# Optimization experiments

Hardware: AMD Instinct MI355X
Metric: run time of the kernel (lower is better)

## Reference

```python
import jax, jax.numpy as jnp
import numpy as np

B, IN_DIM, UNITS = 2048, 256, 512

def setup_inputs() -> dict:
    key = jax.random.key(0)
    k1, k2 = jax.random.split(key)
    x = jax.random.uniform(k1, (B, IN_DIM), dtype=jnp.float32)
    weights = jax.random.uniform(k2, (IN_DIM * UNITS,), dtype=jnp.float32)
    return {"x": x, "weights": weights}

def reference(x, weights):
    # kernel: [in_dim, units]; transpose -> [units, in_dim]
    in_dim = x.shape[-1]
    kT = weights.reshape(in_dim, UNITS).T  # [units, in_dim]
    # broadcast multiply-add: [B, 1, in_dim] * [units, in_dim] + (1 - kT)
    # -> [B, units, in_dim]; product-reduce over in_dim (XOR via bipolar product)
    t = x[:, None, :] * kT + (1.0 - kT)
    return jnp.prod(t, axis=-1)  # [B, units]
```

## Files before the change

### kernel.cpp

```cpp
#include <hip/hip_runtime.h>


typedef float v2f __attribute__((ext_vector_type(2)));

#define B_DIM   2048
#define IN_DIM  256
#define UNITS   512
#define BT      32
#define UT      64
#define BLOCK   256
#define NSL     8
#define KIS     32
#define CHUNK   8
#define NCH     4
#define PSTR    68
#define PLANE   (32*PSTR)

__global__ __launch_bounds__(BLOCK) void prodw_kernel(
    const float* __restrict__ x,
    const float* __restrict__ w,
    float* __restrict__ out)
{
    __shared__ __align__(16) float lds[4 * PLANE];
    float* __restrict__ xs  = lds;
    float* __restrict__ wsb = lds + 2048;

    const int tid = threadIdx.x;
    const int s   = tid >> 5;
    const int t   = tid & 31;
    const int tb  = t >> 3;
    const int tu  = t & 7;
    const int ublk = blockIdx.x * UT;
    const int bblk = blockIdx.y * BT;

    __align__(16) float af[64];
    v2f* __restrict__ acc = (v2f*)af;
#pragma unroll
    for (int k = 0; k < 32; ++k) acc[k] = (v2f){1.0f, 1.0f};

    const int swz = (s & 1) << 2;

    for (int c = 0; c < NCH; ++c) {
        __syncthreads();

#pragma unroll
        for (int r = 0; r < 2; ++r) {
            const int idx  = r * BLOCK + tid;
            const int b    = idx & 31;
            const int srow = idx >> 5;
            const int ss   = srow >> 1;
            const int h    = srow & 1;
            const float4 f = *(const float4*)
                (x + (size_t)(bblk + b) * IN_DIM + ss * KIS + c * CHUNK + h * 4);
            const int row = ss * 8 + h * 4;
            xs[(row + 0) * 32 + b] = f.x;
            xs[(row + 1) * 32 + b] = f.y;
            xs[(row + 2) * 32 + b] = f.z;
            xs[(row + 3) * 32 + b] = f.w;
        }
#pragma unroll
        for (int r = 0; r < 4; ++r) {
            const int idx = r * BLOCK + tid;
            const int row = idx >> 4;
            const int u4  = (idx & 15) * 4;
            const int ss  = row >> 3;
            const int ii  = row & 7;
            const int xr  = (ss & 1) << 2;
            const float4 f = *(const float4*)
                (w + (size_t)(ss * KIS + c * CHUNK + ii) * UNITS + ublk + u4);
            *(float4*)&wsb[row * 64 + (u4 ^ xr)] = f;
        }
        __syncthreads();

#pragma unroll
        for (int ii = 0; ii < CHUNK; ++ii) {
            const int row = s * 8 + ii;
            const float4 xa = *(const float4*)&xs[row * 32 + tb * 8];
            const float4 xb = *(const float4*)&xs[row * 32 + tb * 8 + 4];
            const float4 w0 = *(const float4*)&wsb[row * 64 + ((tu * 8) ^ swz)];
            const float4 w1 = *(const float4*)&wsb[row * 64 + ((tu * 8 + 4) ^ swz)];

            v2f wv[4] = {{w0.x, w0.y}, {w0.z, w0.w}, {w1.x, w1.y}, {w1.z, w1.w}};
            v2f cv[4];
#pragma unroll
            for (int q = 0; q < 4; ++q) cv[q] = (v2f){1.0f, 1.0f} - wv[q];
            const float xv[8] = {xa.x, xa.y, xa.z, xa.w, xb.x, xb.y, xb.z, xb.w};

#pragma unroll
            for (int jb = 0; jb < 8; ++jb) {
                const v2f xbv = {xv[jb], xv[jb]};
#pragma unroll
                for (int q = 0; q < 4; ++q)
                    acc[jb * 4 + q] *= __builtin_elementwise_fma(xbv, wv[q], cv[q]);
            }
        }
    }

#pragma unroll
    for (int half = NSL / 2; half >= 1; half >>= 1) {
        __syncthreads();
        if (s >= half && s < 2 * half) {
            float* __restrict__ pl = lds + (size_t)(s - half) * PLANE + t * PSTR;
#pragma unroll
            for (int k = 0; k < 16; ++k)
                *(float4*)&pl[k * 4] = ((const float4*)af)[k];
        }
        __syncthreads();
        if (s < half) {
            const float* __restrict__ pl = lds + (size_t)s * PLANE + t * PSTR;
#pragma unroll
            for (int k = 0; k < 16; ++k) {
                const float4 q = *(const float4*)&pl[k * 4];
                float4* a4 = &((float4*)af)[k];
                a4->x *= q.x; a4->y *= q.y; a4->z *= q.z; a4->w *= q.w;
            }
        }
    }

    if (s == 0) {
#pragma unroll
        for (int jb = 0; jb < 8; ++jb) {
            float* __restrict__ po =
                out + (size_t)(bblk + tb * 8 + jb) * UNITS + ublk + tu * 8;
            *(float4*)(po)     = *(const float4*)&af[jb * 8];
            *(float4*)(po + 4) = *(const float4*)&af[jb * 8 + 4];
        }
    }
}

extern "C" void kernel_launch(void* const* d_in, const int* in_sizes, int n_in,
                              void* d_out, int out_size, void* d_ws, size_t ws_size,
                              hipStream_t stream) {
    const float* x = (const float*)d_in[0];
    const float* w = (const float*)d_in[1];
    float* out     = (float*)d_out;

    dim3 grid(UNITS / UT, B_DIM / BT);
    prodw_kernel<<<grid, BLOCK, 0, stream>>>(x, w, out);
}
```

Before: 73.19 us.

## Double-buffer weight tiles via async global_load_lds and preload shifted x tile

Weight chunks now go straight from global memory into one of two LDS buffers using async global-to-LDS loads, and the next chunk is prefetched while the current one is computed. The whole x tile for the block is loaded into LDS once, before the loop, with 1 subtracted up front. Each factor then becomes fma(x-1, w, 1), so the per-chunk 1-w computation goes away and the per-chunk barriers drop from two to one. LDS use grows to 64KB per block, which can lower occupancy. Correctness relies on the async LDS writes having finished before the barrier.

```diff
diff --git a/kernel.cpp b/kernel.cpp
--- a/kernel.cpp
+++ b/kernel.cpp
@@ -16,33 +16,51 @@
 #define PSTR    68
 #define PLANE   (32*PSTR)
 
+#define XS_F    (IN_DIM*32)
+#define WBUF_F  (64*64)
+
 __global__ __launch_bounds__(BLOCK) void prodw_kernel(
     const float* __restrict__ x,
     const float* __restrict__ w,
     float* __restrict__ out)
 {
-    __shared__ __align__(16) float lds[4 * PLANE];
+    __shared__ __align__(16) float lds[XS_F + 2 * WBUF_F];
     float* __restrict__ xs  = lds;
-    float* __restrict__ wsb = lds + 2048;
+    float* __restrict__ ws0 = lds + XS_F;
+    float* __restrict__ ws1 = lds + XS_F + WBUF_F;
 
     const int tid = threadIdx.x;
     const int s   = tid >> 5;
     const int t   = tid & 31;
     const int tb  = t >> 3;
     const int tu  = t & 7;
+    const int wv  = tid >> 6;
+    const int ln  = tid & 63;
     const int ublk = blockIdx.x * UT;
     const int bblk = blockIdx.y * BT;
 
-    __align__(16) float af[64];
-    v2f* __restrict__ acc = (v2f*)af;
+    const float* wsrc[4];
+    int lofs[4];
 #pragma unroll
-    for (int k = 0; k < 32; ++k) acc[k] = (v2f){1.0f, 1.0f};
+    for (int k = 0; k < 4; ++k) {
+        const int seg = wv * 4 + k;
+        const int r   = seg * 4 + (ln >> 4);
+        const int ss  = r >> 3;
+        const int ii  = r & 7;
+        const int xr  = (ss & 1) << 2;
+        const int col = ((ln & 15) * 4) ^ xr;
+        wsrc[k] = w + (size_t)(ss * KIS + ii) * UNITS + ublk + col;
+        lofs[k] = seg * 256;
+    }
 
-    const int swz = (s & 1) << 2;
+#pragma unroll
+    for (int k = 0; k < 4; ++k)
+        __builtin_amdgcn_global_load_lds(
+            (const __attribute__((address_space(1))) void*)(wsrc[k]),
+            (__attribute__((address_space(3))) void*)(ws0 + lofs[k]), 16, 0, 0);
 
+#pragma unroll
     for (int c = 0; c < NCH; ++c) {
-        __syncthreads();
-
 #pragma unroll
         for (int r = 0; r < 2; ++r) {
             const int idx  = r * BLOCK + tid;
@@ -52,48 +70,60 @@
             const int h    = srow & 1;
             const float4 f = *(const float4*)
                 (x + (size_t)(bblk + b) * IN_DIM + ss * KIS + c * CHUNK + h * 4);
-            const int row = ss * 8 + h * 4;
-            xs[(row + 0) * 32 + b] = f.x;
-            xs[(row + 1) * 32 + b] = f.y;
-            xs[(row + 2) * 32 + b] = f.z;
-            xs[(row + 3) * 32 + b] = f.w;
+            const int row = ss * KIS + c * CHUNK + h * 4;
+            xs[(row + 0) * 32 + b] = f.x - 1.0f;
+            xs[(row + 1) * 32 + b] = f.y - 1.0f;
+            xs[(row + 2) * 32 + b] = f.z - 1.0f;
+            xs[(row + 3) * 32 + b] = f.w - 1.0f;
         }
+    }
+
+    __align__(16) float af[64];
+    v2f* __restrict__ acc = (v2f*)af;
 #pragma unroll
-        for (int r = 0; r < 4; ++r) {
-            const int idx = r * BLOCK + tid;
-            const int row = idx >> 4;
-            const int u4  = (idx & 15) * 4;
-            const int ss  = row >> 3;
-            const int ii  = row & 7;
-            const int xr  = (ss & 1) << 2;
-            const float4 f = *(const float4*)
-                (w + (size_t)(ss * KIS + c * CHUNK + ii) * UNITS + ublk + u4);
-            *(float4*)&wsb[row * 64 + (u4 ^ xr)] = f;
+    for (int k = 0; k < 32; ++k) acc[k] = (v2f){1.0f, 1.0f};
+
+    const int swz = (s & 1) << 2;
+
+    __syncthreads();
+
+#pragma unroll
+    for (int c = 0; c < NCH; ++c) {
+        float* const wcur = (c & 1) ? ws1 : ws0;
+        float* const wnxt = (c & 1) ? ws0 : ws1;
+
+        if (c + 1 < NCH) {
+            const size_t coff = (size_t)(c + 1) * CHUNK * UNITS;
+#pragma unroll
+            for (int k = 0; k < 4; ++k)
+                __builtin_amdgcn_global_load_lds(
+                    (const __attribute__((address_space(1))) void*)(wsrc[k] + coff),
+                    (__attribute__((address_space(3))) void*)(wnxt + lofs[k]),
+                    16, 0, 0);
         }
-        __syncthreads();
 
 #pragma unroll
         for (int ii = 0; ii < CHUNK; ++ii) {
-            const int row = s * 8 + ii;
-            const float4 xa = *(const float4*)&xs[row * 32 + tb * 8];
-            const float4 xb = *(const float4*)&xs[row * 32 + tb * 8 + 4];
-            const float4 w0 = *(const float4*)&wsb[row * 64 + ((tu * 8) ^ swz)];
-            const float4 w1 = *(const float4*)&wsb[row * 64 + ((tu * 8 + 4) ^ swz)];
+            const int xrow = s * KIS + c * CHUNK + ii;
+            const int wrow = s * CHUNK + ii;
+            const float4 ya = *(const float4*)&xs[xrow * 32 + tb * 8];
+            const float4 yb = *(const float4*)&xs[xrow * 32 + tb * 8 + 4];
+            const float4 w0 = *(const float4*)&wcur[wrow * 64 + ((tu * 8) ^ swz)];
+            const float4 w1 = *(const float4*)&wcur[wrow * 64 + ((tu * 8 + 4) ^ swz)];
 
-            v2f wv[4] = {{w0.x, w0.y}, {w0.z, w0.w}, {w1.x, w1.y}, {w1.z, w1.w}};
-            v2f cv[4];
-#pragma unroll
-            for (int q = 0; q < 4; ++q) cv[q] = (v2f){1.0f, 1.0f} - wv[q];
-            const float xv[8] = {xa.x, xa.y, xa.z, xa.w, xb.x, xb.y, xb.z, xb.w};
+            v2f wvv[4] = {{w0.x, w0.y}, {w0.z, w0.w}, {w1.x, w1.y}, {w1.z, w1.w}};
+            const float yv[8] = {ya.x, ya.y, ya.z, ya.w, yb.x, yb.y, yb.z, yb.w};
 
 #pragma unroll
             for (int jb = 0; jb < 8; ++jb) {
-                const v2f xbv = {xv[jb], xv[jb]};
+                const v2f yy = {yv[jb], yv[jb]};
 #pragma unroll
                 for (int q = 0; q < 4; ++q)
-                    acc[jb * 4 + q] *= __builtin_elementwise_fma(xbv, wv[q], cv[q]);
+                    acc[jb * 4 + q] *= __builtin_elementwise_fma(
+                        yy, wvv[q], (v2f){1.0f, 1.0f});
             }
         }
+        __syncthreads();
     }
 
 #pragma unroll
```

New measurement: 71.76 us. 1.02x faster.

## Use per-wave k-slices with wave-uniform weight loads and fma(w, x-1, 1)

Applied to the files above, without the earlier changes.

Rewrites the kernel so each of 16 waves owns a 16-wide slice of in_dim, with each lane handling one batch row and holding x-1 in registers. Weights are read directly from global memory at wave-uniform addresses (scalar-loadable) instead of being staged through LDS. The factor becomes fma(w, x-1, 1), which removes the per-element 1-w computation. Block size grows to 1024 threads with 64x64 tiles, and a 4-level LDS tree reduction with an XOR swizzle combines the partial products. The trade-off is a larger reduction, fewer blocks, and possible register pressure from 64 accumulators per lane under a 1024-thread launch bound.

```diff
diff --git a/kernel.cpp b/kernel.cpp
--- a/kernel.cpp
+++ b/kernel.cpp
@@ -6,125 +6,82 @@
 #define B_DIM   2048
 #define IN_DIM  256
 #define UNITS   512
-#define BT      32
+#define BT      64
 #define UT      64
-#define BLOCK   256
-#define NSL     8
-#define KIS     32
-#define CHUNK   8
-#define NCH     4
-#define PSTR    68
-#define PLANE   (32*PSTR)
+#define BLOCK   1024
+#define NW      16
+#define KIS     16
+#define PLANE_F (64*64)
 
-__global__ __launch_bounds__(BLOCK) void prodw_kernel(
+__global__ __launch_bounds__(BLOCK, 4) void prodw_kernel(
     const float* __restrict__ x,
     const float* __restrict__ w,
     float* __restrict__ out)
 {
-    __shared__ __align__(16) float lds[4 * PLANE];
-    float* __restrict__ xs  = lds;
-    float* __restrict__ wsb = lds + 2048;
+    __shared__ __align__(16) float lds[(NW / 2) * PLANE_F];
 
-    const int tid = threadIdx.x;
-    const int s   = tid >> 5;
-    const int t   = tid & 31;
-    const int tb  = t >> 3;
-    const int tu  = t & 7;
+    const int tid  = threadIdx.x;
+    const int ln   = tid & 63;
+    const int wid  = __builtin_amdgcn_readfirstlane(tid >> 6);
     const int ublk = blockIdx.x * UT;
     const int bblk = blockIdx.y * BT;
 
-    __align__(16) float af[64];
-    v2f* __restrict__ acc = (v2f*)af;
+    float yv[KIS];
+    {
+        const float* xp = x + (size_t)(bblk + ln) * IN_DIM + wid * KIS;
 #pragma unroll
-    for (int k = 0; k < 32; ++k) acc[k] = (v2f){1.0f, 1.0f};
+        for (int k = 0; k < KIS / 4; ++k) {
+            const float4 f = *(const float4*)(xp + 4 * k);
+            yv[4 * k + 0] = f.x - 1.0f;
+            yv[4 * k + 1] = f.y - 1.0f;
+            yv[4 * k + 2] = f.z - 1.0f;
+            yv[4 * k + 3] = f.w - 1.0f;
+        }
+    }
 
-    const int swz = (s & 1) << 2;
+    v2f acc[32];
+#pragma unroll
+    for (int q = 0; q < 32; ++q) acc[q] = (v2f){1.0f, 1.0f};
 
-    for (int c = 0; c < NCH; ++c) {
-        __syncthreads();
+    const float* wp = w + (size_t)(wid * KIS) * UNITS + ublk;
+
+#pragma unroll 4
+    for (int ii = 0; ii < KIS; ++ii) {
+        const float* wr = wp + (size_t)ii * UNITS;
+        const v2f yy = {yv[ii], yv[ii]};
+#pragma unroll
+        for (int q = 0; q < 32; ++q) {
+            const v2f wv = *(const v2f*)(wr + 2 * q);
+            acc[q] *= __builtin_elementwise_fma(wv, yy, (v2f){1.0f, 1.0f});
+        }
+    }
 
 #pragma unroll
-        for (int r = 0; r < 2; ++r) {
-            const int idx  = r * BLOCK + tid;
-            const int b    = idx & 31;
-            const int srow = idx >> 5;
-            const int ss   = srow >> 1;
-            const int h    = srow & 1;
-            const float4 f = *(const float4*)
-                (x + (size_t)(bblk + b) * IN_DIM + ss * KIS + c * CHUNK + h * 4);
-            const int row = ss * 8 + h * 4;
-            xs[(row + 0) * 32 + b] = f.x;
-            xs[(row + 1) * 32 + b] = f.y;
-            xs[(row + 2) * 32 + b] = f.z;
-            xs[(row + 3) * 32 + b] = f.w;
-        }
+    for (int half = NW / 2; half >= 1; half >>= 1) {
+        __syncthreads();
+        if (wid >= half && wid < 2 * half) {
+            float* pl = lds + (size_t)(wid - half) * PLANE_F + ln * 64;
 #pragma unroll
-        for (int r = 0; r < 4; ++r) {
-            const int idx = r * BLOCK + tid;
-            const int row = idx >> 4;
-            const int u4  = (idx & 15) * 4;
-            const int ss  = row >> 3;
-            const int ii  = row & 7;
-            const int xr  = (ss & 1) << 2;
-            const float4 f = *(const float4*)
-                (w + (size_t)(ss * KIS + c * CHUNK + ii) * UNITS + ublk + u4);
-            *(float4*)&wsb[row * 64 + (u4 ^ xr)] = f;
+            for (int k = 0; k < 16; ++k)
+                *(float4*)&pl[(4 * k) ^ ((ln & 7) << 2)] = ((const float4*)acc)[k];
         }
         __syncthreads();
-
+        if (wid < half) {
+            const float* pl = lds + (size_t)wid * PLANE_F + ln * 64;
 #pragma unroll
-        for (int ii = 0; ii < CHUNK; ++ii) {
-            const int row = s * 8 + ii;
-            const float4 xa = *(const float4*)&xs[row * 32 + tb * 8];
-            const float4 xb = *(const float4*)&xs[row * 32 + tb * 8 + 4];
-            const float4 w0 = *(const float4*)&wsb[row * 64 + ((tu * 8) ^ swz)];
-            const float4 w1 = *(const float4*)&wsb[row * 64 + ((tu * 8 + 4) ^ swz)];
-
-            v2f wv[4] = {{w0.x, w0.y}, {w0.z, w0.w}, {w1.x, w1.y}, {w1.z, w1.w}};
-            v2f cv[4];
-#pragma unroll
-            for (int q = 0; q < 4; ++q) cv[q] = (v2f){1.0f, 1.0f} - wv[q];
-            const float xv[8] = {xa.x, xa.y, xa.z, xa.w, xb.x, xb.y, xb.z, xb.w};
-
-#pragma unroll
-            for (int jb = 0; jb < 8; ++jb) {
-                const v2f xbv = {xv[jb], xv[jb]};
-#pragma unroll
-                for (int q = 0; q < 4; ++q)
-                    acc[jb * 4 + q] *= __builtin_elementwise_fma(xbv, wv[q], cv[q]);
+            for (int k = 0; k < 16; ++k) {
+                const float4 qv = *(const float4*)&pl[(4 * k) ^ ((ln & 7) << 2)];
+                float4* a4 = &((float4*)acc)[k];
+                a4->x *= qv.x; a4->y *= qv.y; a4->z *= qv.z; a4->w *= qv.w;
             }
         }
     }
 
+    if (wid == 0) {
+        float* po = out + (size_t)(bblk + ln) * UNITS + ublk;
 #pragma unroll
-    for (int half = NSL / 2; half >= 1; half >>= 1) {
-        __syncthreads();
-        if (s >= half && s < 2 * half) {
-            float* __restrict__ pl = lds + (size_t)(s - half) * PLANE + t * PSTR;
-#pragma unroll
-            for (int k = 0; k < 16; ++k)
-                *(float4*)&pl[k * 4] = ((const float4*)af)[k];
-        }
-        __syncthreads();
-        if (s < half) {
-            const float* __restrict__ pl = lds + (size_t)s * PLANE + t * PSTR;
-#pragma unroll
-            for (int k = 0; k < 16; ++k) {
-                const float4 q = *(const float4*)&pl[k * 4];
-                float4* a4 = &((float4*)af)[k];
-                a4->x *= q.x; a4->y *= q.y; a4->z *= q.z; a4->w *= q.w;
-            }
-        }
-    }
-
-    if (s == 0) {
-#pragma unroll
-        for (int jb = 0; jb < 8; ++jb) {
-            float* __restrict__ po =
-                out + (size_t)(bblk + tb * 8 + jb) * UNITS + ublk + tu * 8;
-            *(float4*)(po)     = *(const float4*)&af[jb * 8];
-            *(float4*)(po + 4) = *(const float4*)&af[jb * 8 + 4];
-        }
+        for (int k = 0; k < 16; ++k)
+            *(float4*)(po + 4 * k) = ((const float4*)acc)[k];
     }
 }
 
```

After: 71.31 us. -2.6%, faster.
